# Kernel tuning notes

Hardware: AMD Instinct MI355X
Metric: run time of the kernel (lower is better)

Reference implementation:

```python
import jax, jax.numpy as jnp
import numpy as np

K = 1024          # num_embeddings
D = 64            # embedding_dim
BETA = 0.25
B, H, W = 32, 32, 32


def setup_inputs() -> dict:
    key = jax.random.key(0)
    k1, k2 = jax.random.split(key)
    x = jax.random.normal(k1, (B, D, H, W), dtype=jnp.float32)
    # embedding.weight.data.uniform_(-1/K, 1/K)
    emb_w = jax.random.uniform(k2, (K, D), dtype=jnp.float32, minval=-1.0 / K, maxval=1.0 / K)
    return {"x": x, "emb_w": emb_w}


def reference(x, emb_w):
    # x: [B, D, H, W] -> [B, H, W, D]
    xl = jnp.transpose(x, (0, 2, 3, 1))
    latents_shape = xl.shape
    flat = xl.reshape(-1, D)                         # [N, D]
    dist = ((flat ** 2).sum(axis=1, keepdims=True)
            + (emb_w ** 2).sum(axis=1)[None, :]
            - 2.0 * flat @ emb_w.T)
    idx = jnp.argmin(dist, axis=1)                   # [N]
    encoded = jax.nn.one_hot(idx, K, dtype=flat.dtype)  # [N, K]
    # gather (same math as encoded @ emb_w, avoids NxK matmul)
    quantized = emb_w[idx].reshape(latents_shape)    # [B, H, W, D]

    commitment_loss = jnp.mean((jax.lax.stop_gradient(quantized) - xl) ** 2)
    emb_loss = jnp.mean((quantized - jax.lax.stop_gradient(xl)) ** 2)
    vq_loss = commitment_loss + BETA * emb_loss

    # straight-through estimator
    quantized_st = xl + jax.lax.stop_gradient(quantized - xl)

    mean_probs = encoded.mean(axis=0)                # [K]
    perplexity = jnp.exp(-jnp.sum(mean_probs * jnp.log(mean_probs + 1e-10)))

    out = jnp.transpose(quantized_st, (0, 3, 1, 2))  # [B, D, H, W]
    return (out, vq_loss, perplexity, encoded)
```

## Files before the change

kernel.cpp:

```cpp
#include <hip/hip_runtime.h>

#define OUT_OFF_Q 0
#define OUT_OFF_VQ 2097152
#define OUT_OFF_PPL 2097153
#define OUT_OFF_ENC 2097154

typedef __attribute__((ext_vector_type(8))) short short8;
typedef __attribute__((ext_vector_type(4))) float f32x4;

__device__ __forceinline__ unsigned short f2bf(float f) {
    unsigned u = __builtin_bit_cast(unsigned, f);
    u += 0x7fffu + ((u >> 16) & 1u);
    return (unsigned short)(u >> 16);
}
__device__ __forceinline__ float bf2f(unsigned short h) {
    unsigned u = ((unsigned)h) << 16;
    return __builtin_bit_cast(float, u);
}

__global__ __launch_bounds__(64) void vq_prep(
    const float* __restrict__ E, unsigned short* __restrict__ Efrag,
    float* __restrict__ ee, int* __restrict__ counts)
{
    const int t = threadIdx.x;
    const int kt = blockIdx.x;
    const int code = kt * 16 + (t & 15);
    const int q = t >> 4;

    const float* ep0 = E + code * 64 + q * 8;
    const float* ep1 = ep0 + 32;
    short8 ah0, ah1, al0, al1;
    float s = 0.f;
    #pragma unroll
    for (int j = 0; j < 8; ++j) {
        float v0 = ep0[j];
        unsigned short h0 = f2bf(v0);
        ah0[j] = (short)h0;
        al0[j] = (short)f2bf(v0 - bf2f(h0));
        s = fmaf(v0, v0, s);
        float v1 = ep1[j];
        unsigned short h1 = f2bf(v1);
        ah1[j] = (short)h1;
        al1[j] = (short)f2bf(v1 - bf2f(h1));
        s = fmaf(v1, v1, s);
    }
    short8* dst = (short8*)Efrag + (size_t)kt * 256;
    dst[0 * 64 + t] = ah0;
    dst[1 * 64 + t] = ah1;
    dst[2 * 64 + t] = al0;
    dst[3 * 64 + t] = al1;

    s += __shfl_xor(s, 16);
    s += __shfl_xor(s, 32);
    if (t < 16) ee[code] = s;

    const int gid = blockIdx.x * 64 + t;
    if (gid < 1024) counts[gid] = 0;
}

__global__ __launch_bounds__(256, 4) void vq_main(
    const float* __restrict__ X, const float* __restrict__ E,
    const unsigned short* __restrict__ Efrag, const float* __restrict__ ee,
    float* __restrict__ out, int* __restrict__ counts,
    float* __restrict__ lossPart)
{
    __shared__ float s_ee[1024];
    __shared__ float s_val[4][32];
    __shared__ int   s_idx[4][32];
    __shared__ float s_loss[4];

    const int t = threadIdx.x;
    const int l = t & 63;
    const int w = __builtin_amdgcn_readfirstlane(t >> 6);
    const int col = l & 15;
    const int quad = l >> 4;
    const int n0 = blockIdx.x * 32;
    const int b = n0 >> 10;
    const int hwb = n0 & 1023;

    ((float4*)s_ee)[t] = ((const float4*)ee)[t];

    short8 bh[2][2], bl[2][2];
    const float* xb = X + (size_t)b * 65536 + hwb;
    #pragma unroll
    for (int nt = 0; nt < 2; ++nt) {
        const float* xn = xb + nt * 16 + col;
        #pragma unroll
        for (int ks = 0; ks < 2; ++ks) {
            short8 vh, vl;
            #pragma unroll
            for (int j = 0; j < 8; ++j) {
                float v = xn[(size_t)(ks * 32 + quad * 8 + j) * 1024];
                unsigned short hb = f2bf(v);
                vh[j] = (short)hb;
                vl[j] = (short)f2bf(v - bf2f(hb));
            }
            bh[nt][ks] = vh;
            bl[nt][ks] = vl;
        }
    }

    __syncthreads();

    float best[2] = {3.4e38f, 3.4e38f};
    int   bidx[2] = {0, 0};
    const short8* fw = (const short8*)Efrag + (size_t)(w * 16) * 256;
    #pragma unroll 2
    for (int kt = 0; kt < 16; ++kt) {
        const int kb = w * 256 + kt * 16;
        const short8* fb = fw + (size_t)kt * 256;
        short8 ah0 = fb[0 * 64 + l];
        short8 ah1 = fb[1 * 64 + l];
        short8 al0 = fb[2 * 64 + l];
        short8 al1 = fb[3 * 64 + l];
        f32x4 eev = *((const f32x4*)&s_ee[kb + quad * 4]);
        #pragma unroll
        for (int nt = 0; nt < 2; ++nt) {
            f32x4 c = {0.f, 0.f, 0.f, 0.f};
            c = __builtin_amdgcn_mfma_f32_16x16x32_bf16(ah0, bh[nt][0], c, 0, 0, 0);
            c = __builtin_amdgcn_mfma_f32_16x16x32_bf16(ah1, bh[nt][1], c, 0, 0, 0);
            c = __builtin_amdgcn_mfma_f32_16x16x32_bf16(al0, bh[nt][0], c, 0, 0, 0);
            c = __builtin_amdgcn_mfma_f32_16x16x32_bf16(al1, bh[nt][1], c, 0, 0, 0);
            c = __builtin_amdgcn_mfma_f32_16x16x32_bf16(ah0, bl[nt][0], c, 0, 0, 0);
            c = __builtin_amdgcn_mfma_f32_16x16x32_bf16(ah1, bl[nt][1], c, 0, 0, 0);
            #pragma unroll
            for (int r = 0; r < 4; ++r) {
                float val = fmaf(-2.f, c[r], eev[r]);
                int k = kb + quad * 4 + r;
                if (val < best[nt]) { best[nt] = val; bidx[nt] = k; }
            }
        }
    }

    #pragma unroll
    for (int nt = 0; nt < 2; ++nt) {
        float v = best[nt]; int i = bidx[nt];
        float ov = __shfl_xor(v, 16); int oi = __shfl_xor(i, 16);
        if (ov < v || (ov == v && oi < i)) { v = ov; i = oi; }
        ov = __shfl_xor(v, 32); oi = __shfl_xor(i, 32);
        if (ov < v || (ov == v && oi < i)) { v = ov; i = oi; }
        best[nt] = v; bidx[nt] = i;
    }
    if (quad < 2) {
        s_val[w][quad * 16 + col] = best[quad];
        s_idx[w][quad * 16 + col] = bidx[quad];
    }
    __syncthreads();

    if (t < 32) {
        float fv = s_val[0][t]; int fi0 = s_idx[0][t];
        #pragma unroll
        for (int j = 1; j < 4; ++j) {
            float v = s_val[j][t]; int i = s_idx[j][t];
            if (v < fv || (v == fv && i < fi0)) { fv = v; fi0 = i; }
        }
        s_idx[0][t] = fi0;
        atomicAdd(&counts[fi0], 1);
    }
    __syncthreads();

    {
        const int nl = l & 31;
        const int half = l >> 5;
        const int fi = s_idx[0][nl];
        const int hw = hwb + nl;
        const int d0 = (w << 4) + (half << 3);
        const float* er = E + ((size_t)fi << 6) + d0;
        float4 g0 = *(const float4*)(er);
        float4 g1 = *(const float4*)(er + 4);
        float q[8] = {g0.x, g0.y, g0.z, g0.w, g1.x, g1.y, g1.z, g1.w};
        float* op = out + OUT_OFF_Q + (size_t)b * 65536 + hw;
        const float* xp = X + (size_t)b * 65536 + hw;
        float lsum = 0.f;
        #pragma unroll
        for (int dd = 0; dd < 8; ++dd) {
            const int d = d0 + dd;
            op[(size_t)d * 1024] = q[dd];
            float diff = q[dd] - xp[(size_t)d * 1024];
            lsum = fmaf(diff, diff, lsum);
        }
        #pragma unroll
        for (int off = 32; off; off >>= 1) lsum += __shfl_down(lsum, off);
        if (l == 0) s_loss[w] = lsum;
    }
    __syncthreads();
    if (t == 0)
        lossPart[blockIdx.x] = s_loss[0] + s_loss[1] + s_loss[2] + s_loss[3];

    {
        f32x4* enc = (f32x4*)(out + OUT_OFF_ENC);
        const int rbase = w << 3;
        for (int rr = 0; rr < 8; ++rr) {
            const int r = rbase + rr;
            const int ridx = s_idx[0][r];
            f32x4* erow = enc + (size_t)(n0 + r) * 256;
            #pragma unroll
            for (int c4 = 0; c4 < 4; ++c4) {
                const int kb4 = (c4 << 8) + (l << 2);
                f32x4 v = {0.f, 0.f, 0.f, 0.f};
                const int dlt = ridx - kb4;
                if (dlt == 0) v.x = 1.f;
                else if (dlt == 1) v.y = 1.f;
                else if (dlt == 2) v.z = 1.f;
                else if (dlt == 3) v.w = 1.f;
                erow[(c4 << 6) + l] = v;
            }
        }
    }
}

__global__ __launch_bounds__(1024) void vq_finalize(
    const int* __restrict__ counts, const float* __restrict__ lossPart,
    float* __restrict__ out)
{
    __shared__ float redp[16];
    __shared__ float redl[16];
    const int t = threadIdx.x;
    const float p = (float)counts[t] * (1.0f / 32768.0f);
    float v = p * logf(p + 1e-10f);
    float ls = lossPart[t];
    #pragma unroll
    for (int off = 32; off; off >>= 1) {
        v += __shfl_down(v, off);
        ls += __shfl_down(ls, off);
    }
    if ((t & 63) == 0) { redp[t >> 6] = v; redl[t >> 6] = ls; }
    __syncthreads();
    if (t == 0) {
        float s = 0.f, sl = 0.f;
        #pragma unroll
        for (int i = 0; i < 16; ++i) { s += redp[i]; sl += redl[i]; }
        out[OUT_OFF_PPL] = expf(-s);
        out[OUT_OFF_VQ] = 1.25f * sl * (1.0f / 2097152.0f);
    }
}

extern "C" void kernel_launch(void* const* d_in, const int* in_sizes, int n_in,
                              void* d_out, int out_size, void* d_ws, size_t ws_size,
                              hipStream_t stream) {
    const float* X = (const float*)d_in[0];
    const float* E = (const float*)d_in[1];
    float* out = (float*)d_out;

    int* counts = (int*)d_ws;
    float* lossPart = (float*)((char*)d_ws + 4096);
    float* ee = (float*)((char*)d_ws + 8192);
    unsigned short* Efrag = (unsigned short*)((char*)d_ws + 12288);

    vq_prep<<<64, 64, 0, stream>>>(E, Efrag, ee, counts);
    vq_main<<<1024, 256, 0, stream>>>(X, E, Efrag, ee, out, counts, lossPart);
    vq_finalize<<<1, 1024, 0, stream>>>(counts, lossPart, out);
}
```

Baseline: 168.7 us.

## Give each wave 16 rows and full codebook, drop cross-wave LDS reduction

Each wave now owns 16 input rows and scans all 1024 codes itself, instead of four waves splitting the codebook across 32 shared rows. This removes the shared-memory staging of code norms, the cross-wave argmin reduction and most block barriers, and the grid halves to 512 blocks with per-wave loss partials. In exchange, each wave streams the whole codebook fragment set from global/L2, which is four times more B-fragment traffic per row, and the 16-row tile no longer reuses each A-fragment across two row tiles.

```diff
diff --git a/kernel.cpp b/kernel.cpp
--- a/kernel.cpp
+++ b/kernel.cpp
@@ -64,116 +64,82 @@
     float* __restrict__ out, int* __restrict__ counts,
     float* __restrict__ lossPart)
 {
-    __shared__ float s_ee[1024];
-    __shared__ float s_val[4][32];
-    __shared__ int   s_idx[4][32];
-    __shared__ float s_loss[4];
-
     const int t = threadIdx.x;
     const int l = t & 63;
-    const int w = __builtin_amdgcn_readfirstlane(t >> 6);
+    const int w = t >> 6;
     const int col = l & 15;
     const int quad = l >> 4;
-    const int n0 = blockIdx.x * 32;
+    const int n0 = blockIdx.x * 64 + w * 16;
     const int b = n0 >> 10;
     const int hwb = n0 & 1023;
 
-    ((float4*)s_ee)[t] = ((const float4*)ee)[t];
-
-    short8 bh[2][2], bl[2][2];
-    const float* xb = X + (size_t)b * 65536 + hwb;
+    short8 bh[2], bl[2];
+    const float* xn = X + (size_t)b * 65536 + hwb + col;
     #pragma unroll
-    for (int nt = 0; nt < 2; ++nt) {
-        const float* xn = xb + nt * 16 + col;
-        #pragma unroll
-        for (int ks = 0; ks < 2; ++ks) {
-            short8 vh, vl;
-            #pragma unroll
-            for (int j = 0; j < 8; ++j) {
-                float v = xn[(size_t)(ks * 32 + quad * 8 + j) * 1024];
-                unsigned short hb = f2bf(v);
-                vh[j] = (short)hb;
-                vl[j] = (short)f2bf(v - bf2f(hb));
-            }
-            bh[nt][ks] = vh;
-            bl[nt][ks] = vl;
-        }
-    }
-
-    __syncthreads();
-
-    float best[2] = {3.4e38f, 3.4e38f};
-    int   bidx[2] = {0, 0};
-    const short8* fw = (const short8*)Efrag + (size_t)(w * 16) * 256;
-    #pragma unroll 2
-    for (int kt = 0; kt < 16; ++kt) {
-        const int kb = w * 256 + kt * 16;
-        const short8* fb = fw + (size_t)kt * 256;
+    for (int ks = 0; ks < 2; ++ks) {
+        short8 vh, vl;
+        #pragma unroll
+        for (int j = 0; j < 8; ++j) {
+            float v = xn[(size_t)(ks * 32 + quad * 8 + j) * 1024];
+            unsigned short hb = f2bf(v);
+            vh[j] = (short)hb;
+            vl[j] = (short)f2bf(v - bf2f(hb));
+        }
+        bh[ks] = vh;
+        bl[ks] = vl;
+    }
+
+    float best = 3.4e38f;
+    int   bidx = 0;
+    const short8* fr = (const short8*)Efrag;
+    #pragma unroll 4
+    for (int kt = 0; kt < 64; ++kt) {
+        const int kb = kt * 16;
+        const short8* fb = fr + (size_t)kt * 256;
         short8 ah0 = fb[0 * 64 + l];
         short8 ah1 = fb[1 * 64 + l];
         short8 al0 = fb[2 * 64 + l];
         short8 al1 = fb[3 * 64 + l];
-        f32x4 eev = *((const f32x4*)&s_ee[kb + quad * 4]);
-        #pragma unroll
-        for (int nt = 0; nt < 2; ++nt) {
-            f32x4 c = {0.f, 0.f, 0.f, 0.f};
-            c = __builtin_amdgcn_mfma_f32_16x16x32_bf16(ah0, bh[nt][0], c, 0, 0, 0);
-            c = __builtin_amdgcn_mfma_f32_16x16x32_bf16(ah1, bh[nt][1], c, 0, 0, 0);
-            c = __builtin_amdgcn_mfma_f32_16x16x32_bf16(al0, bh[nt][0], c, 0, 0, 0);
-            c = __builtin_amdgcn_mfma_f32_16x16x32_bf16(al1, bh[nt][1], c, 0, 0, 0);
-            c = __builtin_amdgcn_mfma_f32_16x16x32_bf16(ah0, bl[nt][0], c, 0, 0, 0);
-            c = __builtin_amdgcn_mfma_f32_16x16x32_bf16(ah1, bl[nt][1], c, 0, 0, 0);
-            #pragma unroll
-            for (int r = 0; r < 4; ++r) {
-                float val = fmaf(-2.f, c[r], eev[r]);
-                int k = kb + quad * 4 + r;
-                if (val < best[nt]) { best[nt] = val; bidx[nt] = k; }
-            }
-        }
-    }
-
-    #pragma unroll
-    for (int nt = 0; nt < 2; ++nt) {
-        float v = best[nt]; int i = bidx[nt];
-        float ov = __shfl_xor(v, 16); int oi = __shfl_xor(i, 16);
-        if (ov < v || (ov == v && oi < i)) { v = ov; i = oi; }
-        ov = __shfl_xor(v, 32); oi = __shfl_xor(i, 32);
-        if (ov < v || (ov == v && oi < i)) { v = ov; i = oi; }
-        best[nt] = v; bidx[nt] = i;
-    }
-    if (quad < 2) {
-        s_val[w][quad * 16 + col] = best[quad];
-        s_idx[w][quad * 16 + col] = bidx[quad];
-    }
-    __syncthreads();
-
-    if (t < 32) {
-        float fv = s_val[0][t]; int fi0 = s_idx[0][t];
-        #pragma unroll
-        for (int j = 1; j < 4; ++j) {
-            float v = s_val[j][t]; int i = s_idx[j][t];
-            if (v < fv || (v == fv && i < fi0)) { fv = v; fi0 = i; }
-        }
-        s_idx[0][t] = fi0;
-        atomicAdd(&counts[fi0], 1);
-    }
-    __syncthreads();
+        f32x4 eev = *((const f32x4*)(ee + kb + quad * 4));
+        f32x4 c = {0.f, 0.f, 0.f, 0.f};
+        c = __builtin_amdgcn_mfma_f32_16x16x32_bf16(ah0, bh[0], c, 0, 0, 0);
+        c = __builtin_amdgcn_mfma_f32_16x16x32_bf16(ah1, bh[1], c, 0, 0, 0);
+        c = __builtin_amdgcn_mfma_f32_16x16x32_bf16(al0, bh[0], c, 0, 0, 0);
+        c = __builtin_amdgcn_mfma_f32_16x16x32_bf16(al1, bh[1], c, 0, 0, 0);
+        c = __builtin_amdgcn_mfma_f32_16x16x32_bf16(ah0, bl[0], c, 0, 0, 0);
+        c = __builtin_amdgcn_mfma_f32_16x16x32_bf16(ah1, bl[1], c, 0, 0, 0);
+        #pragma unroll
+        for (int r = 0; r < 4; ++r) {
+            float val = fmaf(-2.f, c[r], eev[r]);
+            int k = kb + quad * 4 + r;
+            if (val < best) { best = val; bidx = k; }
+        }
+    }
 
     {
-        const int nl = l & 31;
-        const int half = l >> 5;
-        const int fi = s_idx[0][nl];
-        const int hw = hwb + nl;
-        const int d0 = (w << 4) + (half << 3);
+        float ov = __shfl_xor(best, 16); int oi = __shfl_xor(bidx, 16);
+        if (ov < best || (ov == best && oi < bidx)) { best = ov; bidx = oi; }
+        ov = __shfl_xor(best, 32); oi = __shfl_xor(bidx, 32);
+        if (ov < best || (ov == best && oi < bidx)) { best = ov; bidx = oi; }
+    }
+
+    if (quad == 0) atomicAdd(&counts[bidx], 1);
+
+    {
+        const int fi = bidx;
+        const int d0 = quad << 4;
         const float* er = E + ((size_t)fi << 6) + d0;
         float4 g0 = *(const float4*)(er);
         float4 g1 = *(const float4*)(er + 4);
-        float q[8] = {g0.x, g0.y, g0.z, g0.w, g1.x, g1.y, g1.z, g1.w};
-        float* op = out + OUT_OFF_Q + (size_t)b * 65536 + hw;
-        const float* xp = X + (size_t)b * 65536 + hw;
+        float4 g2 = *(const float4*)(er + 8);
+        float4 g3 = *(const float4*)(er + 12);
+        float q[16] = {g0.x, g0.y, g0.z, g0.w, g1.x, g1.y, g1.z, g1.w,
+                       g2.x, g2.y, g2.z, g2.w, g3.x, g3.y, g3.z, g3.w};
+        float* op = out + OUT_OFF_Q + (size_t)b * 65536 + hwb + col;
+        const float* xp = X + (size_t)b * 65536 + hwb + col;
         float lsum = 0.f;
         #pragma unroll
-        for (int dd = 0; dd < 8; ++dd) {
+        for (int dd = 0; dd < 16; ++dd) {
             const int d = d0 + dd;
             op[(size_t)d * 1024] = q[dd];
             float diff = q[dd] - xp[(size_t)d * 1024];
@@ -181,19 +147,15 @@
         }
         #pragma unroll
         for (int off = 32; off; off >>= 1) lsum += __shfl_down(lsum, off);
-        if (l == 0) s_loss[w] = lsum;
-    }
-    __syncthreads();
-    if (t == 0)
-        lossPart[blockIdx.x] = s_loss[0] + s_loss[1] + s_loss[2] + s_loss[3];
+        if (l == 0) lossPart[blockIdx.x * 4 + w] = lsum;
+    }
 
     {
         f32x4* enc = (f32x4*)(out + OUT_OFF_ENC);
-        const int rbase = w << 3;
-        for (int rr = 0; rr < 8; ++rr) {
-            const int r = rbase + rr;
-            const int ridx = s_idx[0][r];
-            f32x4* erow = enc + (size_t)(n0 + r) * 256;
+        #pragma unroll 4
+        for (int rr = 0; rr < 16; ++rr) {
+            const int ridx = __shfl(bidx, rr);
+            f32x4* erow = enc + (size_t)(n0 + rr) * 256;
             #pragma unroll
             for (int c4 = 0; c4 < 4; ++c4) {
                 const int kb4 = (c4 << 8) + (l << 2);
@@ -218,7 +180,7 @@
     const int t = threadIdx.x;
     const float p = (float)counts[t] * (1.0f / 32768.0f);
     float v = p * logf(p + 1e-10f);
-    float ls = lossPart[t];
+    float ls = lossPart[t] + lossPart[t + 1024];
     #pragma unroll
     for (int off = 32; off; off >>= 1) {
         v += __shfl_down(v, off);
@@ -244,10 +206,10 @@
 
     int* counts = (int*)d_ws;
     float* lossPart = (float*)((char*)d_ws + 4096);
-    float* ee = (float*)((char*)d_ws + 8192);
-    unsigned short* Efrag = (unsigned short*)((char*)d_ws + 12288);
+    float* ee = (float*)((char*)d_ws + 16384);
+    unsigned short* Efrag = (unsigned short*)((char*)d_ws + 20480);
 
     vq_prep<<<64, 64, 0, stream>>>(E, Efrag, ee, counts);
-    vq_main<<<1024, 256, 0, stream>>>(X, E, Efrag, ee, out, counts, lossPart);
+    vq_main<<<512, 256, 0, stream>>>(X, E, Efrag, ee, out, counts, lossPart);
     vq_finalize<<<1, 1024, 0, stream>>>(counts, lossPart, out);
 }
```

Measured after the change: 186.0 us. 10.3% more time.
